# Kernel tuning notes

Measured on AMD Instinct MI355X. Metric: run time of the kernel, lower is better.

Reference implementation:

```python
import jax, jax.numpy as jnp
import numpy as np

V, D, NH, L, T, B = 32000, 1024, 16, 6, 1024, 2
HS = D // NH
EPS = 1e-5


def setup_inputs() -> dict:
    key = jax.random.key(0)
    ks = jax.random.split(key, 20)
    s = 0.02
    inp = {
        'tokens': jax.random.randint(ks[0], (B, T), 0, V),
        'tok_emb': jax.random.normal(ks[1], (V, D), jnp.float32) * s,
        'pos_emb': jax.random.normal(ks[2], (T, D), jnp.float32) * s,
        'Wq': jax.random.normal(ks[3], (L, D, NH, HS), jnp.float32) * s,
        'Wk': jax.random.normal(ks[4], (L, D, NH, HS), jnp.float32) * s,
        'Wv': jax.random.normal(ks[5], (L, D, NH, HS), jnp.float32) * s,
        'Wo': jax.random.normal(ks[6], (L, D, D), jnp.float32) * s,
        'bo': jnp.zeros((L, D), jnp.float32),
        'ln1_s': jnp.ones((L, D), jnp.float32),
        'ln1_b': jnp.zeros((L, D), jnp.float32),
        'ln2_s': jnp.ones((L, D), jnp.float32),
        'ln2_b': jnp.zeros((L, D), jnp.float32),
        'W1': jax.random.normal(ks[7], (L, D, 4 * D), jnp.float32) * s,
        'b1': jnp.zeros((L, 4 * D), jnp.float32),
        'W2': jax.random.normal(ks[8], (L, 4 * D, D), jnp.float32) * s,
        'b2': jnp.zeros((L, D), jnp.float32),
        'lnf_s': jnp.ones((D,), jnp.float32),
        'lnf_b': jnp.zeros((D,), jnp.float32),
        'Wlm': jax.random.normal(ks[9], (D, V), jnp.float32) * s,
        'blm': jnp.zeros((V,), jnp.float32),
    }
    return inp


def _layernorm(x, scale, bias):
    m = jnp.mean(x, axis=-1, keepdims=True)
    v = jnp.mean(jnp.square(x - m), axis=-1, keepdims=True)
    return (x - m) * jax.lax.rsqrt(v + EPS) * scale + bias


def reference(tokens, tok_emb, pos_emb, Wq, Wk, Wv, Wo, bo,
              ln1_s, ln1_b, ln2_s, ln2_b, W1, b1, W2, b2,
              lnf_s, lnf_b, Wlm, blm):
    x = tok_emb[tokens] + pos_emb[None, :, :]  # [B,T,D]
    causal = jnp.tril(jnp.ones((T, T), bool))
    scale = HS ** -0.5
    for l in range(L):
        h = _layernorm(x, ln1_s[l], ln1_b[l])
        q = jnp.einsum('btd,dhe->bhte', h, Wq[l])
        k = jnp.einsum('btd,dhe->bhte', h, Wk[l])
        v = jnp.einsum('btd,dhe->bhte', h, Wv[l])
        wei = jnp.einsum('bhqe,bhke->bhqk', q, k) * scale
        wei = jnp.where(causal, wei, -jnp.inf)
        wei = jax.nn.softmax(wei, axis=-1)
        attn = jnp.einsum('bhqk,bhke->bhqe', wei, v)  # [B,NH,T,HS]
        attn = attn.transpose(0, 2, 1, 3).reshape(B, T, D)
        x = x + attn @ Wo[l] + bo[l]
        h = _layernorm(x, ln2_s[l], ln2_b[l])
        x = x + jax.nn.relu(h @ W1[l] + b1[l]) @ W2[l] + b2[l]
    x = _layernorm(x, lnf_s, lnf_b)
    logits = x @ Wlm + blm  # [B,T,V]
    return logits
```

## Files before the change

### kernel.cpp

```cpp
#include <hip/hip_runtime.h>
#include <hip/hip_bf16.h>
#include <stdint.h>

#define L_LAYERS 6
#define D_MODEL  1024
#define N_HEAD   16
#define H_SZ     64
#define T_SEQ    1024
#define B_BATCH  2
#define M_ROWS   2048
#define V_VOCAB  32000

typedef __attribute__((ext_vector_type(8))) short bf16x8;
typedef __attribute__((ext_vector_type(4))) short bf16x4;
typedef __attribute__((ext_vector_type(4))) float floatx4;

static __device__ __forceinline__ short f2bf(float f) {
  __hip_bfloat16 h = __float2bfloat16(f);
  return *reinterpret_cast<short*>(&h);
}

static __device__ __forceinline__ void lds_cp16(const void* g, void* l) {
  __builtin_amdgcn_global_load_lds(
      (const __attribute__((address_space(1))) uint32_t*)g,
      (__attribute__((address_space(3))) uint32_t*)l, 16, 0, 0);
}

#define WVM(n) asm volatile("s_waitcnt vmcnt(" #n ")" ::: "memory")
#define BARR __builtin_amdgcn_s_barrier()

__global__ __launch_bounds__(256) void transpose_cvt(const float* __restrict__ in,
                                                     short* __restrict__ out,
                                                     int R, int C,
                                                     long in_stride, long out_stride) {
  in  += (size_t)blockIdx.z * in_stride;
  out += (size_t)blockIdx.z * out_stride;
  __shared__ float tile[64][65];
  int rt = blockIdx.x, ct = blockIdx.y;
  int tid = threadIdx.x;
  int r0 = tid >> 4;
  int c0 = (tid & 15) << 2;
  const float* ip = in + (size_t)(rt * 64) * C + ct * 64;
#pragma unroll
  for (int p = 0; p < 4; ++p) {
    int r = r0 + (p << 4);
    float4 v = *(const float4*)(ip + (size_t)r * C + c0);
    tile[r][c0] = v.x; tile[r][c0 + 1] = v.y; tile[r][c0 + 2] = v.z; tile[r][c0 + 3] = v.w;
  }
  __syncthreads();
  short* op = out + (size_t)(ct * 64) * R + rt * 64;
#pragma unroll
  for (int p = 0; p < 4; ++p) {
    int c = r0 + (p << 4);
    bf16x4 s;
    s.x = f2bf(tile[c0 + 0][c]);
    s.y = f2bf(tile[c0 + 1][c]);
    s.z = f2bf(tile[c0 + 2][c]);
    s.w = f2bf(tile[c0 + 3][c]);
    *(bf16x4*)(op + (size_t)c * R + c0) = s;
  }
}

__global__ __launch_bounds__(256) void embed_kernel(const int* __restrict__ tokens,
                                                    const float* __restrict__ tok_emb,
                                                    const float* __restrict__ pos_emb,
                                                    float* __restrict__ x) {
  int row = blockIdx.x;
  int t = row & 1023;
  int tok = tokens[row];
  int c = threadIdx.x << 2;
  float4 e = *(const float4*)(tok_emb + (size_t)tok * 1024 + c);
  float4 p = *(const float4*)(pos_emb + (size_t)t * 1024 + c);
  float4 rr; rr.x = e.x + p.x; rr.y = e.y + p.y; rr.z = e.z + p.z; rr.w = e.w + p.w;
  *(float4*)(x + (size_t)row * 1024 + c) = rr;
}

__global__ __launch_bounds__(256) void ln_kernel(const float* __restrict__ xin,
                                                 const float* __restrict__ sc,
                                                 const float* __restrict__ bi,
                                                 short* __restrict__ out) {
  int row = blockIdx.x, tid = threadIdx.x;
  int c = tid << 2;
  float4 v = *(const float4*)(xin + (size_t)row * 1024 + c);
  float s = v.x + v.y + v.z + v.w;
  float q = v.x * v.x + v.y * v.y + v.z * v.z + v.w * v.w;
#pragma unroll
  for (int off = 32; off > 0; off >>= 1) {
    s += __shfl_xor(s, off);
    q += __shfl_xor(q, off);
  }
  __shared__ float rs[4], rq[4];
  if ((tid & 63) == 0) { rs[tid >> 6] = s; rq[tid >> 6] = q; }
  __syncthreads();
  s = rs[0] + rs[1] + rs[2] + rs[3];
  q = rq[0] + rq[1] + rq[2] + rq[3];
  float mean = s * (1.f / 1024.f);
  float var = q * (1.f / 1024.f) - mean * mean;
  float rstd = rsqrtf(var + 1e-5f);
  float4 g = *(const float4*)(sc + c);
  float4 bb = *(const float4*)(bi + c);
  bf16x4 o4;
  o4.x = f2bf((v.x - mean) * rstd * g.x + bb.x);
  o4.y = f2bf((v.y - mean) * rstd * g.y + bb.y);
  o4.z = f2bf((v.z - mean) * rstd * g.z + bb.z);
  o4.w = f2bf((v.w - mean) * rstd * g.w + bb.w);
  *(bf16x4*)(out + (size_t)row * 1024 + c) = o4;
}

template <bool BIAS, bool RELU, bool RESID, bool OUTBF16>
__global__ __launch_bounds__(256) void gemm3_kernel(const short* __restrict__ A,
                                                    const short* __restrict__ Bt,
                                                    const float* __restrict__ bias,
                                                    const float* __restrict__ resid,
                                                    void* __restrict__ Cout,
                                                    int K, int N) {
  constexpr int ABY = 64 * 128;
  constexpr int BBY = 128 * 128;
  extern __shared__ char smem[];
  char* Asm = smem;
  char* Bsm = smem + 3 * ABY;
  const int NB = N >> 7;
  int nwg = 32 * NB;
  int bid = blockIdx.x;
  int wgid = (bid & 7) * (nwg >> 3) + (bid >> 3);
  int bn = wgid >> 5, bm = wgid & 31;
  int tid = threadIdx.x;
  int lane = tid & 63, w = tid >> 6;
  int lr = lane & 15, lg = lane >> 4;
  int wn = w & 1, wm = w >> 1;

  const floatx4 FZ = {0.f, 0.f, 0.f, 0.f};
  floatx4 acc[2][4];
#pragma unroll
  for (int m = 0; m < 2; ++m)
#pragma unroll
    for (int n = 0; n < 4; ++n) acc[m][n] = FZ;

  size_t aoff[2], boff[4];
  {
    int rr = tid >> 3;
    int g = (tid & 7) ^ (rr & 7);
#pragma unroll
    for (int i = 0; i < 2; ++i)
      aoff[i] = (size_t)(bm * 64 + i * 32 + rr) * K + g * 8;
#pragma unroll
    for (int i = 0; i < 4; ++i)
      boff[i] = (size_t)(bn * 128 + i * 32 + rr) * K + g * 8;
  }

#define STA3(b, k0)                                                        \
  _Pragma("unroll") for (int i = 0; i < 2; ++i)                            \
    lds_cp16(A + aoff[i] + (k0), Asm + (b) * ABY + i * 4096 + tid * 16);
#define STB3(b, k0)                                                        \
  _Pragma("unroll") for (int i = 0; i < 4; ++i)                            \
    lds_cp16(Bt + boff[i] + (k0), Bsm + (b) * BBY + i * 4096 + tid * 16);
#define LDA3(b, kh)                                                        \
  _Pragma("unroll") for (int f = 0; f < 2; ++f) {                          \
    int lrow = wm * 32 + f * 16 + lr;                                      \
    af[f] = *(const bf16x8*)(Asm + (b) * ABY + lrow * 128 +                \
                             (((((kh) << 2) + lg) ^ (lrow & 7)) << 4));    \
  }
#define LDB3(b, kh)                                                        \
  _Pragma("unroll") for (int n = 0; n < 4; ++n) {                          \
    int lcol = wn * 64 + n * 16 + lr;                                      \
    bfr[n] = *(const bf16x8*)(Bsm + (b) * BBY + lcol * 128 +               \
                              (((((kh) << 2) + lg) ^ (lcol & 7)) << 4));   \
  }
#define MFMA3                                                              \
  __builtin_amdgcn_s_setprio(1);                                           \
  _Pragma("unroll") for (int f = 0; f < 2; ++f)                            \
  _Pragma("unroll") for (int n = 0; n < 4; ++n)                            \
    acc[f][n] = __builtin_amdgcn_mfma_f32_16x16x32_bf16(af[f], bfr[n],     \
                                                        acc[f][n], 0, 0, 0);\
  __builtin_amdgcn_s_setprio(0);

  const int nt = K >> 6;
  STA3(0, 0); STB3(0, 0);
  STA3(1, 64); STB3(1, 64);
  WVM(6);
  BARR;

  int cbuf = 0, sbuf = 2;
  for (int t = 0; t < nt; ++t) {
    bf16x8 af[2], bfr[4];
    bool pre = (t + 2 < nt);
    int k2 = (t + 2) << 6;
    if (pre) { STA3(sbuf, k2); }
    LDA3(cbuf, 0); LDB3(cbuf, 0);
    MFMA3;
    if (pre) { STB3(sbuf, k2); }
    LDA3(cbuf, 1); LDB3(cbuf, 1);
    MFMA3;
    if (pre) { WVM(6); } else { WVM(0); }
    BARR;
    cbuf = (cbuf == 2) ? 0 : cbuf + 1;
    sbuf = (sbuf == 2) ? 0 : sbuf + 1;
  }

#pragma unroll
  for (int n = 0; n < 4; ++n) {
    int col = (bn << 7) + wn * 64 + (n << 4) + lr;
    float bv = 0.f;
    if (BIAS) bv = bias[col];
#pragma unroll
    for (int m = 0; m < 2; ++m) {
      int row0 = bm * 64 + wm * 32 + (m << 4) + (lg << 2);
#pragma unroll
      for (int r = 0; r < 4; ++r) {
        size_t idx = (size_t)(row0 + r) * N + col;
        float val = acc[m][n][r] + bv;
        if (RESID) val += resid[idx];
        if (RELU) val = fmaxf(val, 0.f);
        if (OUTBF16) ((short*)Cout)[idx] = f2bf(val);
        else ((float*)Cout)[idx] = val;
      }
    }
  }
#undef STA3
#undef STB3
#undef LDA3
#undef LDB3
#undef MFMA3
}

template <bool BIAS, bool OUTBF16>
__global__ __launch_bounds__(512) void gemm8_kernel(const short* __restrict__ A,
                                                    const short* __restrict__ Bt,
                                                    const float* __restrict__ bias,
                                                    void* __restrict__ Cout,
                                                    int K, int N) {
  extern __shared__ char smem[];
  char* Asm = smem;
  char* Bsm = smem + 65536;
  const int NB = N >> 8;
  int nwg = 8 * NB;
  int bid = blockIdx.x;
  int wgid = (bid & 7) * (nwg >> 3) + (bid >> 3);
  int bm = wgid & 7, bn = wgid >> 3;
  int tid = threadIdx.x;
  int lane = tid & 63, w = tid >> 6;
  int lr = lane & 15, lg = lane >> 4;
  int wm = w >> 2, wn = w & 3;

  const floatx4 FZ = {0.f, 0.f, 0.f, 0.f};
  floatx4 acc[8][4];
#pragma unroll
  for (int m = 0; m < 8; ++m)
#pragma unroll
    for (int n = 0; n < 4; ++n) acc[m][n] = FZ;

  size_t aoff[2][2], boff[4];
  {
    int rr = tid >> 3;
    int g = (tid & 7) ^ (rr & 7);
#pragma unroll
    for (int c = 0; c < 2; ++c)
#pragma unroll
      for (int i = 0; i < 2; ++i) {
        int lrow = i * 64 + rr;
        int grow = (lrow & 63) + ((lrow >> 6) << 7) + (c << 6);
        aoff[c][i] = (size_t)(bm * 256 + grow) * K + g * 8;
      }
#pragma unroll
    for (int i = 0; i < 4; ++i)
      boff[i] = (size_t)(bn * 256 + i * 64 + rr) * K + g * 8;
  }

  bf16x8 areg[4], breg[2][4];

#define LDA8(chunk, kh)                                                          \
  _Pragma("unroll") for (int f = 0; f < 4; ++f) {                                \
    int lrow = wm * 64 + f * 16 + lr;                                            \
    areg[f] = *(const bf16x8*)(Asm + buf * 32768 + (chunk) * 16384 + lrow * 128  \
                               + (((((kh) << 2) + lg) ^ (lrow & 7)) << 4));      \
  }
#define LDB8(kh)                                                                 \
  _Pragma("unroll") for (int n = 0; n < 4; ++n) {                                \
    int lcol = wn * 64 + n * 16 + lr;                                            \
    breg[kh][n] = *(const bf16x8*)(Bsm + buf * 32768 + lcol * 128                \
                                   + (((((kh) << 2) + lg) ^ (lcol & 7)) << 4));  \
  }
#define MFMA16(mh, kh)                                                           \
  __builtin_amdgcn_s_setprio(1);                                                 \
  _Pragma("unroll") for (int f = 0; f < 4; ++f)                                  \
  _Pragma("unroll") for (int n = 0; n < 4; ++n)                                  \
    acc[(mh) * 4 + f][n] = __builtin_amdgcn_mfma_f32_16x16x32_bf16(              \
        areg[f], breg[kh][n], acc[(mh) * 4 + f][n], 0, 0, 0);                    \
  __builtin_amdgcn_s_setprio(0);
#define STA8(chunk, dstbuf, k0)                                                  \
  _Pragma("unroll") for (int i = 0; i < 2; ++i)                                  \
    lds_cp16(A + aoff[chunk][i] + (k0),                                          \
             Asm + (dstbuf) * 32768 + (chunk) * 16384 + i * 8192 + tid * 16);
#define STB8(dstbuf, k0)                                                         \
  _Pragma("unroll") for (int i = 0; i < 4; ++i)                                  \
    lds_cp16(Bt + boff[i] + (k0),                                                \
             Bsm + (dstbuf) * 32768 + i * 8192 + tid * 16);

  const int nt = K >> 6;
  STA8(0, 0, 0); STB8(0, 0); STA8(1, 0, 0);
  WVM(2);
  BARR;

  int buf = 0;
  for (int t = 0; t < nt - 1; ++t) {
    int k1 = (t + 1) << 6;
    int ob = buf ^ 1;
    LDA8(0, 0); LDB8(0);
    STA8(0, ob, k1);
    BARR;
    MFMA16(0, 0);
    BARR;
    LDA8(0, 1); LDB8(1);
    STB8(ob, k1);
    WVM(6);
    BARR;
    MFMA16(0, 1);
    BARR;
    LDA8(1, 0);
    STA8(1, ob, k1);
    BARR;
    MFMA16(1, 0);
    BARR;
    LDA8(1, 1);
    WVM(2);
    BARR;
    MFMA16(1, 1);
    BARR;
    buf ^= 1;
  }
  LDA8(0, 0); LDB8(0);
  MFMA16(0, 0);
  LDA8(0, 1); LDB8(1);
  MFMA16(0, 1);
  WVM(0);
  BARR;
  LDA8(1, 0);
  MFMA16(1, 0);
  LDA8(1, 1);
  MFMA16(1, 1);

#pragma unroll
  for (int n = 0; n < 4; ++n) {
    int col = (bn << 8) + (wn << 6) + (n << 4) + lr;
    float bv = 0.f;
    if (BIAS) bv = bias[col];
#pragma unroll
    for (int m = 0; m < 8; ++m) {
      int row0 = (bm << 8) + (wm << 7) + (m << 4) + (lg << 2);
#pragma unroll
      for (int r = 0; r < 4; ++r) {
        size_t idx = (size_t)(row0 + r) * N + col;
        float val = acc[m][n][r] + bv;
        if (OUTBF16) ((short*)Cout)[idx] = f2bf(val);
        else ((float*)Cout)[idx] = val;
      }
    }
  }
#undef LDA8
#undef LDB8
#undef MFMA16
#undef STA8
#undef STB8
}

__global__ __launch_bounds__(256) void vt_kernel(const short* __restrict__ qkv,
                                                 short* __restrict__ vt) {
  int bh = blockIdx.x, tt = blockIdx.y;
  int b = bh >> 4, hh = bh & 15;
  __shared__ short tile[64][68];
  int tid = threadIdx.x;
  int r0 = tid >> 4;
  int c4 = (tid & 15) << 2;
  const short* ip = qkv + (size_t)((b << 10) + (tt << 6)) * 3072 + 2048 + (hh << 6);
#pragma unroll
  for (int p = 0; p < 4; ++p) {
    int t = r0 + (p << 4);
    bf16x4 v = *(const bf16x4*)(ip + (size_t)t * 3072 + c4);
    tile[t][c4] = v.x; tile[t][c4 + 1] = v.y; tile[t][c4 + 2] = v.z; tile[t][c4 + 3] = v.w;
  }
  __syncthreads();
  short* op = vt + (size_t)(bh << 6) * 1024 + (tt << 6);
#pragma unroll
  for (int p = 0; p < 4; ++p) {
    int e = r0 + (p << 4);
    bf16x4 sv;
    sv.x = tile[c4 + 0][e];
    sv.y = tile[c4 + 1][e];
    sv.z = tile[c4 + 2][e];
    sv.w = tile[c4 + 3][e];
    *(bf16x4*)(op + (size_t)e * 1024 + c4) = sv;
  }
}

__global__ __launch_bounds__(256) void attn_kernel(const short* __restrict__ qkv,
                                                   const short* __restrict__ vt,
                                                   short* __restrict__ out) {
  int bh = blockIdx.x;
  int qt = blockIdx.y;
  int b = bh >> 4, hh = bh & 15;
  int tid = threadIdx.x;
  int lane = tid & 63, w = tid >> 6;
  int lr = lane & 15, lg = lane >> 4;

  __shared__ short Ks[64 * 64];
  __shared__ short Vs[64 * 64];
  __shared__ short Ps[4][16 * 68];

  const floatx4 FZ = {0.f, 0.f, 0.f, 0.f};
  const short* qb = qkv + (size_t)((b << 10) + (qt << 6) + (w << 4) + lr) * 3072 + (hh << 6);
  bf16x8 qf0 = *(const bf16x8*)(qb + (lg << 3));
  bf16x8 qf1 = *(const bf16x8*)(qb + 32 + (lg << 3));

  floatx4 o[4];
  float mrun[4], lrun[4];
#pragma unroll
  for (int r = 0; r < 4; ++r) { o[r] = FZ; mrun[r] = -3e38f; lrun[r] = 0.f; }

  int sr = lane >> 3;
  int cb = (lane & 7) << 4;
  int csw = cb ^ (sr << 4);
  const short* kB = qkv + (size_t)(b << 10) * 3072 + 1024 + (hh << 6);
  const short* vB = vt + (size_t)(bh << 6) * 1024;

  for (int jt = 0; jt <= qt; ++jt) {
    __syncthreads();
#pragma unroll
    for (int j = 0; j < 2; ++j) {
      int ch = w * 2 + j;
      int row = (ch << 3) + sr;
      lds_cp16(kB + (size_t)((jt << 6) + row) * 3072 + (csw >> 1), (short*)Ks + (ch << 9));
      lds_cp16(vB + (size_t)row * 1024 + (jt << 6) + (csw >> 1), (short*)Vs + (ch << 9));
    }
    __syncthreads();

    const char* KsB = (const char*)Ks;
    const char* VsB = (const char*)Vs;
    floatx4 s[4];
#pragma unroll
    for (int f = 0; f < 4; ++f) {
      int rk = (f << 4) + lr;
      int sw = (rk & 7) << 4;
      bf16x8 kf0 = *(const bf16x8*)(KsB + rk * 128 + ((lg << 4) ^ sw));
      bf16x8 kf1 = *(const bf16x8*)(KsB + rk * 128 + ((64 + (lg << 4)) ^ sw));
      floatx4 t = __builtin_amdgcn_mfma_f32_16x16x32_bf16(qf0, kf0, FZ, 0, 0, 0);
      s[f] = __builtin_amdgcn_mfma_f32_16x16x32_bf16(qf1, kf1, t, 0, 0, 0);
    }

    float p[4][4], mt[4];
    bool diag = (jt == qt);
    int rowloc = (w << 4) + (lg << 2);
#pragma unroll
    for (int r = 0; r < 4; ++r) {
      float m = -3e38f;
#pragma unroll
      for (int f = 0; f < 4; ++f) {
        float sv = s[f][r] * 0.125f;
        if (diag && ((f << 4) + lr > rowloc + r)) sv = -3e38f;
        p[f][r] = sv;
        m = fmaxf(m, sv);
      }
      mt[r] = m;
    }
#pragma unroll
    for (int off = 1; off < 16; off <<= 1) {
#pragma unroll
      for (int r = 0; r < 4; ++r) mt[r] = fmaxf(mt[r], __shfl_xor(mt[r], off));
    }
    float corr[4], psum[4];
#pragma unroll
    for (int r = 0; r < 4; ++r) {
      float mnew = fmaxf(mrun[r], mt[r]);
      corr[r] = __expf(mrun[r] - mnew);
      mrun[r] = mnew;
      float ps = 0.f;
#pragma unroll
      for (int f = 0; f < 4; ++f) {
        float e = __expf(p[f][r] - mnew);
        p[f][r] = e;
        ps += e;
      }
      psum[r] = ps;
    }
#pragma unroll
    for (int off = 1; off < 16; off <<= 1) {
#pragma unroll
      for (int r = 0; r < 4; ++r) psum[r] += __shfl_xor(psum[r], off);
    }
    floatx4 cv;
#pragma unroll
    for (int r = 0; r < 4; ++r) { lrun[r] = lrun[r] * corr[r] + psum[r]; cv[r] = corr[r]; }
#pragma unroll
    for (int f = 0; f < 4; ++f) o[f] *= cv;

    char* PsB = (char*)&Ps[w][0];
#pragma unroll
    for (int f = 0; f < 4; ++f)
#pragma unroll
      for (int r = 0; r < 4; ++r)
        *(short*)(PsB + ((lg << 2) + r) * 136 + (((f << 4) + lr) << 1)) = f2bf(p[f][r]);

#pragma unroll
    for (int kk = 0; kk < 2; ++kk) {
      const char* pb = PsB + lr * 136 + (kk << 6) + (lg << 4);
      union { struct { bf16x4 lo, hi; } h2; bf16x8 v; } pu;
      pu.h2.lo = *(const bf16x4*)pb;
      pu.h2.hi = *(const bf16x4*)(pb + 8);
      bf16x8 pa = pu.v;
#pragma unroll
      for (int f = 0; f < 4; ++f) {
        int rv = (f << 4) + lr;
        int sw = (rv & 7) << 4;
        bf16x8 vf = *(const bf16x8*)(VsB + rv * 128 + ((((kk << 6)) + (lg << 4)) ^ sw));
        o[f] = __builtin_amdgcn_mfma_f32_16x16x32_bf16(pa, vf, o[f], 0, 0, 0);
      }
    }
  }

#pragma unroll
  for (int f = 0; f < 4; ++f) {
#pragma unroll
    for (int r = 0; r < 4; ++r) {
      int row = (qt << 6) + (w << 4) + (lg << 2) + r;
      int col = (hh << 6) + (f << 4) + lr;
      out[(size_t)((b << 10) + row) * 1024 + col] = f2bf(o[f][r] / lrun[r]);
    }
  }
}

extern "C" void kernel_launch(void* const* d_in, const int* in_sizes, int n_in,
                              void* d_out, int out_size, void* d_ws, size_t ws_size,
                              hipStream_t stream) {
  const int*   tokens  = (const int*)d_in[0];
  const float* tok_emb = (const float*)d_in[1];
  const float* pos_emb = (const float*)d_in[2];
  const float* Wq  = (const float*)d_in[3];
  const float* Wk  = (const float*)d_in[4];
  const float* Wv  = (const float*)d_in[5];
  const float* Wo  = (const float*)d_in[6];
  const float* bo  = (const float*)d_in[7];
  const float* ln1s = (const float*)d_in[8];
  const float* ln1b = (const float*)d_in[9];
  const float* ln2s = (const float*)d_in[10];
  const float* ln2b = (const float*)d_in[11];
  const float* W1  = (const float*)d_in[12];
  const float* b1  = (const float*)d_in[13];
  const float* W2  = (const float*)d_in[14];
  const float* b2  = (const float*)d_in[15];
  const float* lnfs = (const float*)d_in[16];
  const float* lnfb = (const float*)d_in[17];
  const float* Wlm = (const float*)d_in[18];
  const float* blm = (const float*)d_in[19];

  short* wqkvT = (short*)d_ws;
  short* woT   = wqkvT + (size_t)L_LAYERS * 3072 * 1024;
  short* w1T   = woT   + (size_t)L_LAYERS * 1024 * 1024;
  short* w2T   = w1T   + (size_t)L_LAYERS * 4096 * 1024;
  short* wlmT  = w2T   + (size_t)L_LAYERS * 1024 * 4096;
  float* x     = (float*)(wlmT + (size_t)V_VOCAB * 1024);
  short* h     = (short*)(x + (size_t)M_ROWS * 1024);
  short* qkv   = h + (size_t)M_ROWS * 1024;
  short* vtb   = qkv + (size_t)M_ROWS * 3072;
  short* attnb = vtb + (size_t)B_BATCH * N_HEAD * H_SZ * T_SEQ;
  short* mid   = attnb + (size_t)M_ROWS * 1024;

  dim3 blk(256, 1, 1);

  (void)hipFuncSetAttribute(reinterpret_cast<const void*>(&gemm8_kernel<true, false>),
                            hipFuncAttributeMaxDynamicSharedMemorySize, 131072);
  (void)hipFuncSetAttribute(reinterpret_cast<const void*>(&gemm3_kernel<false, false, false, true>),
                            hipFuncAttributeMaxDynamicSharedMemorySize, 73728);
  (void)hipFuncSetAttribute(reinterpret_cast<const void*>(&gemm3_kernel<true, false, true, false>),
                            hipFuncAttributeMaxDynamicSharedMemorySize, 73728);
  (void)hipFuncSetAttribute(reinterpret_cast<const void*>(&gemm3_kernel<true, true, false, true>),
                            hipFuncAttributeMaxDynamicSharedMemorySize, 73728);

  transpose_cvt<<<dim3(16, 16, 6), blk, 0, stream>>>(Wq, wqkvT,             1024, 1024, 1048576, 3072 * 1024);
  transpose_cvt<<<dim3(16, 16, 6), blk, 0, stream>>>(Wk, wqkvT + 1048576,   1024, 1024, 1048576, 3072 * 1024);
  transpose_cvt<<<dim3(16, 16, 6), blk, 0, stream>>>(Wv, wqkvT + 2097152,   1024, 1024, 1048576, 3072 * 1024);
  transpose_cvt<<<dim3(16, 16, 6), blk, 0, stream>>>(Wo, woT,               1024, 1024, 1048576, 1048576);
  transpose_cvt<<<dim3(16, 64, 6), blk, 0, stream>>>(W1, w1T,               1024, 4096, 4194304, 4194304);
  transpose_cvt<<<dim3(64, 16, 6), blk, 0, stream>>>(W2, w2T,               4096, 1024, 4194304, 4194304);
  transpose_cvt<<<dim3(16, 500, 1), blk, 0, stream>>>(Wlm, wlmT,            1024, V_VOCAB, 0, 0);

  embed_kernel<<<M_ROWS, blk, 0, stream>>>(tokens, tok_emb, pos_emb, x);

  for (int l = 0; l < L_LAYERS; ++l) {
    ln_kernel<<<M_ROWS, blk, 0, stream>>>(x, ln1s + l * 1024, ln1b + l * 1024, h);
    gemm3_kernel<false, false, false, true><<<32 * 24, blk, 73728, stream>>>(
        h, wqkvT + (size_t)l * 3072 * 1024, nullptr, nullptr, qkv, 1024, 3072);
    vt_kernel<<<dim3(32, 16), blk, 0, stream>>>(qkv, vtb);
    attn_kernel<<<dim3(32, 16), blk, 0, stream>>>(qkv, vtb, attnb);
    gemm3_kernel<true, false, true, false><<<32 * 8, blk, 73728, stream>>>(
        attnb, woT + (size_t)l * 1048576, bo + l * 1024, x, x, 1024, 1024);
    ln_kernel<<<M_ROWS, blk, 0, stream>>>(x, ln2s + l * 1024, ln2b + l * 1024, h);
    gemm3_kernel<true, true, false, true><<<32 * 32, blk, 73728, stream>>>(
        h, w1T + (size_t)l * 4194304, b1 + l * 4096, nullptr, mid, 1024, 4096);
    gemm3_kernel<true, false, true, false><<<32 * 8, blk, 73728, stream>>>(
        mid, w2T + (size_t)l * 4194304, b2 + l * 1024, x, x, 4096, 1024);
  }

  ln_kernel<<<M_ROWS, blk, 0, stream>>>(x, lnfs, lnfb, h);
  gemm8_kernel<true, false><<<dim3(8 * 125), dim3(512, 1, 1), 131072, stream>>>(
      h, wlmT, blm, (float*)d_out, 1024, V_VOCAB);
}
```

Before: 1.210 ms.

## Split-K narrow GEMMs, fuse residual reduce into layernorm, fold V transpose into QKV

The N=1024 GEMMs (Wo, W2), which previously launched only 256 workgroups, now use a two-way split-K kernel that writes fp32 partial sums. A new kernel adds both partials, the bias and the residual, then applies layernorm in one pass. Embedding is fused with the first layernorm, and the QKV GEMM epilogue writes V directly in transposed layout, which removes the separate transpose kernel. The GEMM K-tile is also halved to 32 to cut LDS use and raise occupancy. The cost is extra fp32 partial-buffer traffic and more barriers per unit of work.

```diff
diff --git a/kernel.cpp b/kernel.cpp
--- a/kernel.cpp
+++ b/kernel.cpp
@@ -61,27 +61,21 @@
   }
 }
 
-__global__ __launch_bounds__(256) void embed_kernel(const int* __restrict__ tokens,
-                                                    const float* __restrict__ tok_emb,
-                                                    const float* __restrict__ pos_emb,
-                                                    float* __restrict__ x) {
-  int row = blockIdx.x;
+__global__ __launch_bounds__(256) void embedln_kernel(const int* __restrict__ tokens,
+                                                      const float* __restrict__ tok_emb,
+                                                      const float* __restrict__ pos_emb,
+                                                      float* __restrict__ x,
+                                                      const float* __restrict__ sc,
+                                                      const float* __restrict__ bi,
+                                                      short* __restrict__ out) {
+  int row = blockIdx.x, tid = threadIdx.x;
   int t = row & 1023;
   int tok = tokens[row];
-  int c = threadIdx.x << 2;
+  int c = tid << 2;
   float4 e = *(const float4*)(tok_emb + (size_t)tok * 1024 + c);
   float4 p = *(const float4*)(pos_emb + (size_t)t * 1024 + c);
-  float4 rr; rr.x = e.x + p.x; rr.y = e.y + p.y; rr.z = e.z + p.z; rr.w = e.w + p.w;
-  *(float4*)(x + (size_t)row * 1024 + c) = rr;
-}
-
-__global__ __launch_bounds__(256) void ln_kernel(const float* __restrict__ xin,
-                                                 const float* __restrict__ sc,
-                                                 const float* __restrict__ bi,
-                                                 short* __restrict__ out) {
-  int row = blockIdx.x, tid = threadIdx.x;
-  int c = tid << 2;
-  float4 v = *(const float4*)(xin + (size_t)row * 1024 + c);
+  float4 v; v.x = e.x + p.x; v.y = e.y + p.y; v.z = e.z + p.z; v.w = e.w + p.w;
+  *(float4*)(x + (size_t)row * 1024 + c) = v;
   float s = v.x + v.y + v.z + v.w;
   float q = v.x * v.x + v.y * v.y + v.z * v.z + v.w * v.w;
 #pragma unroll
@@ -107,15 +101,59 @@
   *(bf16x4*)(out + (size_t)row * 1024 + c) = o4;
 }
 
-template <bool BIAS, bool RELU, bool RESID, bool OUTBF16>
-__global__ __launch_bounds__(256) void gemm3_kernel(const short* __restrict__ A,
-                                                    const short* __restrict__ Bt,
-                                                    const float* __restrict__ bias,
-                                                    const float* __restrict__ resid,
-                                                    void* __restrict__ Cout,
-                                                    int K, int N) {
-  constexpr int ABY = 64 * 128;
-  constexpr int BBY = 128 * 128;
+__global__ __launch_bounds__(256) void lnred_kernel(float* __restrict__ xio,
+                                                    const float* __restrict__ P0,
+                                                    const float* __restrict__ P1,
+                                                    const float* __restrict__ gb,
+                                                    const float* __restrict__ sc,
+                                                    const float* __restrict__ bi,
+                                                    short* __restrict__ out) {
+  int row = blockIdx.x, tid = threadIdx.x;
+  int c = tid << 2;
+  size_t base = (size_t)row * 1024 + c;
+  float4 v = *(const float4*)(xio + base);
+  float4 p0 = *(const float4*)(P0 + base);
+  float4 p1 = *(const float4*)(P1 + base);
+  float4 gv = *(const float4*)(gb + c);
+  v.x += p0.x + p1.x + gv.x;
+  v.y += p0.y + p1.y + gv.y;
+  v.z += p0.z + p1.z + gv.z;
+  v.w += p0.w + p1.w + gv.w;
+  *(float4*)(xio + base) = v;
+  float s = v.x + v.y + v.z + v.w;
+  float q = v.x * v.x + v.y * v.y + v.z * v.z + v.w * v.w;
+#pragma unroll
+  for (int off = 32; off > 0; off >>= 1) {
+    s += __shfl_xor(s, off);
+    q += __shfl_xor(q, off);
+  }
+  __shared__ float rs[4], rq[4];
+  if ((tid & 63) == 0) { rs[tid >> 6] = s; rq[tid >> 6] = q; }
+  __syncthreads();
+  s = rs[0] + rs[1] + rs[2] + rs[3];
+  q = rq[0] + rq[1] + rq[2] + rq[3];
+  float mean = s * (1.f / 1024.f);
+  float var = q * (1.f / 1024.f) - mean * mean;
+  float rstd = rsqrtf(var + 1e-5f);
+  float4 g = *(const float4*)(sc + c);
+  float4 bb = *(const float4*)(bi + c);
+  bf16x4 o4;
+  o4.x = f2bf((v.x - mean) * rstd * g.x + bb.x);
+  o4.y = f2bf((v.y - mean) * rstd * g.y + bb.y);
+  o4.z = f2bf((v.z - mean) * rstd * g.z + bb.z);
+  o4.w = f2bf((v.w - mean) * rstd * g.w + bb.w);
+  *(bf16x4*)(out + (size_t)row * 1024 + c) = o4;
+}
+
+template <bool BIAS, bool RELU, bool OUTBF16, bool VSPLIT>
+__global__ __launch_bounds__(256, 4) void gemm3_kernel(const short* __restrict__ A,
+                                                       const short* __restrict__ Bt,
+                                                       const float* __restrict__ bias,
+                                                       void* __restrict__ Cout,
+                                                       short* __restrict__ vtb,
+                                                       int K, int N) {
+  constexpr int ABY = 64 * 64;
+  constexpr int BBY = 128 * 64;
   extern __shared__ char smem[];
   char* Asm = smem;
   char* Bsm = smem + 3 * ABY;
@@ -136,35 +174,31 @@
 #pragma unroll
     for (int n = 0; n < 4; ++n) acc[m][n] = FZ;
 
-  size_t aoff[2], boff[4];
+  size_t aoff, boff[2];
   {
-    int rr = tid >> 3;
-    int g = (tid & 7) ^ (rr & 7);
+    int rr = tid >> 2;
+    int g = (tid & 3) ^ (rr & 3);
+    aoff = (size_t)(bm * 64 + rr) * K + g * 8;
 #pragma unroll
     for (int i = 0; i < 2; ++i)
-      aoff[i] = (size_t)(bm * 64 + i * 32 + rr) * K + g * 8;
-#pragma unroll
-    for (int i = 0; i < 4; ++i)
-      boff[i] = (size_t)(bn * 128 + i * 32 + rr) * K + g * 8;
-  }
-
-#define STA3(b, k0)                                                        \
+      boff[i] = (size_t)(bn * 128 + i * 64 + rr) * K + g * 8;
+  }
+
+#define STA3(b, k0) lds_cp16(A + aoff + (k0), Asm + (b) * ABY + tid * 16);
+#define STB3(b, k0)                                                        \
   _Pragma("unroll") for (int i = 0; i < 2; ++i)                            \
-    lds_cp16(A + aoff[i] + (k0), Asm + (b) * ABY + i * 4096 + tid * 16);
-#define STB3(b, k0)                                                        \
-  _Pragma("unroll") for (int i = 0; i < 4; ++i)                            \
     lds_cp16(Bt + boff[i] + (k0), Bsm + (b) * BBY + i * 4096 + tid * 16);
-#define LDA3(b, kh)                                                        \
+#define LDA3(b)                                                            \
   _Pragma("unroll") for (int f = 0; f < 2; ++f) {                          \
     int lrow = wm * 32 + f * 16 + lr;                                      \
-    af[f] = *(const bf16x8*)(Asm + (b) * ABY + lrow * 128 +                \
-                             (((((kh) << 2) + lg) ^ (lrow & 7)) << 4));    \
-  }
-#define LDB3(b, kh)                                                        \
+    af[f] = *(const bf16x8*)(Asm + (b) * ABY + lrow * 64 +                 \
+                             ((lg ^ (lrow & 3)) << 4));                    \
+  }
+#define LDB3(b)                                                            \
   _Pragma("unroll") for (int n = 0; n < 4; ++n) {                          \
     int lcol = wn * 64 + n * 16 + lr;                                      \
-    bfr[n] = *(const bf16x8*)(Bsm + (b) * BBY + lcol * 128 +               \
-                              (((((kh) << 2) + lg) ^ (lcol & 7)) << 4));   \
+    bfr[n] = *(const bf16x8*)(Bsm + (b) * BBY + lcol * 64 +                \
+                              ((lg ^ (lcol & 3)) << 4));                   \
   }
 #define MFMA3                                                              \
   __builtin_amdgcn_s_setprio(1);                                           \
@@ -174,24 +208,21 @@
                                                         acc[f][n], 0, 0, 0);\
   __builtin_amdgcn_s_setprio(0);
 
-  const int nt = K >> 6;
+  const int nt = K >> 5;
   STA3(0, 0); STB3(0, 0);
-  STA3(1, 64); STB3(1, 64);
-  WVM(6);
+  STA3(1, 32); STB3(1, 32);
+  WVM(3);
   BARR;
 
   int cbuf = 0, sbuf = 2;
   for (int t = 0; t < nt; ++t) {
     bf16x8 af[2], bfr[4];
     bool pre = (t + 2 < nt);
-    int k2 = (t + 2) << 6;
-    if (pre) { STA3(sbuf, k2); }
-    LDA3(cbuf, 0); LDB3(cbuf, 0);
+    int k2 = (t + 2) << 5;
+    if (pre) { STA3(sbuf, k2); STB3(sbuf, k2); }
+    LDA3(cbuf); LDB3(cbuf);
     MFMA3;
-    if (pre) { STB3(sbuf, k2); }
-    LDA3(cbuf, 1); LDB3(cbuf, 1);
-    MFMA3;
-    if (pre) { WVM(6); } else { WVM(0); }
+    if (pre) { WVM(3); } else { WVM(0); }
     BARR;
     cbuf = (cbuf == 2) ? 0 : cbuf + 1;
     sbuf = (sbuf == 2) ? 0 : sbuf + 1;
@@ -205,15 +236,127 @@
 #pragma unroll
     for (int m = 0; m < 2; ++m) {
       int row0 = bm * 64 + wm * 32 + (m << 4) + (lg << 2);
-#pragma unroll
-      for (int r = 0; r < 4; ++r) {
-        size_t idx = (size_t)(row0 + r) * N + col;
-        float val = acc[m][n][r] + bv;
-        if (RESID) val += resid[idx];
-        if (RELU) val = fmaxf(val, 0.f);
-        if (OUTBF16) ((short*)Cout)[idx] = f2bf(val);
-        else ((float*)Cout)[idx] = val;
+      if (VSPLIT && col >= 2048) {
+        int hc = col - 2048;
+        int b = row0 >> 10, t4 = row0 & 1023;
+        ushort4 pk;
+        pk.x = (unsigned short)f2bf(acc[m][n][0]);
+        pk.y = (unsigned short)f2bf(acc[m][n][1]);
+        pk.z = (unsigned short)f2bf(acc[m][n][2]);
+        pk.w = (unsigned short)f2bf(acc[m][n][3]);
+        *(ushort4*)(vtb + ((size_t)(((b << 4) + (hc >> 6)) << 6) + (hc & 63)) * 1024 + t4) = pk;
+      } else {
+#pragma unroll
+        for (int r = 0; r < 4; ++r) {
+          size_t idx = (size_t)(row0 + r) * N + col;
+          float val = acc[m][n][r] + bv;
+          if (RELU) val = fmaxf(val, 0.f);
+          if (OUTBF16) ((short*)Cout)[idx] = f2bf(val);
+          else ((float*)Cout)[idx] = val;
+        }
       }
+    }
+  }
+#undef STA3
+#undef STB3
+#undef LDA3
+#undef LDB3
+#undef MFMA3
+}
+
+__global__ __launch_bounds__(256, 4) void gemm3sk_kernel(const short* __restrict__ A,
+                                                         const short* __restrict__ Bt,
+                                                         float* __restrict__ Pout,
+                                                         int K, int N) {
+  constexpr int ABY = 64 * 64;
+  constexpr int BBY = 128 * 64;
+  extern __shared__ char smem[];
+  char* Asm = smem;
+  char* Bsm = smem + 3 * ABY;
+  const int NB = N >> 7;
+  int nwg = 64 * NB;
+  int bid = blockIdx.x;
+  int wgid = (bid & 7) * (nwg >> 3) + (bid >> 3);
+  int half = wgid >= (nwg >> 1);
+  int w2 = wgid - half * (nwg >> 1);
+  int bn = w2 >> 5, bm = w2 & 31;
+  int kbase = half * (K >> 1);
+  Pout += (size_t)half * M_ROWS * N;
+  int tid = threadIdx.x;
+  int lane = tid & 63, w = tid >> 6;
+  int lr = lane & 15, lg = lane >> 4;
+  int wn = w & 1, wm = w >> 1;
+
+  const floatx4 FZ = {0.f, 0.f, 0.f, 0.f};
+  floatx4 acc[2][4];
+#pragma unroll
+  for (int m = 0; m < 2; ++m)
+#pragma unroll
+    for (int n = 0; n < 4; ++n) acc[m][n] = FZ;
+
+  size_t aoff, boff[2];
+  {
+    int rr = tid >> 2;
+    int g = (tid & 3) ^ (rr & 3);
+    aoff = (size_t)(bm * 64 + rr) * K + kbase + g * 8;
+#pragma unroll
+    for (int i = 0; i < 2; ++i)
+      boff[i] = (size_t)(bn * 128 + i * 64 + rr) * K + kbase + g * 8;
+  }
+
+#define STA3(b, k0) lds_cp16(A + aoff + (k0), Asm + (b) * ABY + tid * 16);
+#define STB3(b, k0)                                                        \
+  _Pragma("unroll") for (int i = 0; i < 2; ++i)                            \
+    lds_cp16(Bt + boff[i] + (k0), Bsm + (b) * BBY + i * 4096 + tid * 16);
+#define LDA3(b)                                                            \
+  _Pragma("unroll") for (int f = 0; f < 2; ++f) {                          \
+    int lrow = wm * 32 + f * 16 + lr;                                      \
+    af[f] = *(const bf16x8*)(Asm + (b) * ABY + lrow * 64 +                 \
+                             ((lg ^ (lrow & 3)) << 4));                    \
+  }
+#define LDB3(b)                                                            \
+  _Pragma("unroll") for (int n = 0; n < 4; ++n) {                          \
+    int lcol = wn * 64 + n * 16 + lr;                                      \
+    bfr[n] = *(const bf16x8*)(Bsm + (b) * BBY + lcol * 64 +                \
+                              ((lg ^ (lcol & 3)) << 4));                   \
+  }
+#define MFMA3                                                              \
+  __builtin_amdgcn_s_setprio(1);                                           \
+  _Pragma("unroll") for (int f = 0; f < 2; ++f)                            \
+  _Pragma("unroll") for (int n = 0; n < 4; ++n)                            \
+    acc[f][n] = __builtin_amdgcn_mfma_f32_16x16x32_bf16(af[f], bfr[n],     \
+                                                        acc[f][n], 0, 0, 0);\
+  __builtin_amdgcn_s_setprio(0);
+
+  const int nt = (K >> 1) >> 5;
+  STA3(0, 0); STB3(0, 0);
+  STA3(1, 32); STB3(1, 32);
+  WVM(3);
+  BARR;
+
+  int cbuf = 0, sbuf = 2;
+  for (int t = 0; t < nt; ++t) {
+    bf16x8 af[2], bfr[4];
+    bool pre = (t + 2 < nt);
+    int k2 = (t + 2) << 5;
+    if (pre) { STA3(sbuf, k2); STB3(sbuf, k2); }
+    LDA3(cbuf); LDB3(cbuf);
+    MFMA3;
+    if (pre) { WVM(3); } else { WVM(0); }
+    BARR;
+    cbuf = (cbuf == 2) ? 0 : cbuf + 1;
+    sbuf = (sbuf == 2) ? 0 : sbuf + 1;
+  }
+
+#pragma unroll
+  for (int n = 0; n < 4; ++n) {
+    int col = (bn << 7) + wn * 64 + (n << 4) + lr;
+#pragma unroll
+    for (int m = 0; m < 2; ++m) {
+      int row0 = bm * 64 + wm * 32 + (m << 4) + (lg << 2);
+#pragma unroll
+      for (int r = 0; r < 4; ++r)
+        Pout[(size_t)(row0 + r) * N + col] = acc[m][n][r];
     }
   }
 #undef STA3
@@ -361,35 +504,6 @@
 #undef MFMA16
 #undef STA8
 #undef STB8
-}
-
-__global__ __launch_bounds__(256) void vt_kernel(const short* __restrict__ qkv,
-                                                 short* __restrict__ vt) {
-  int bh = blockIdx.x, tt = blockIdx.y;
-  int b = bh >> 4, hh = bh & 15;
-  __shared__ short tile[64][68];
-  int tid = threadIdx.x;
-  int r0 = tid >> 4;
-  int c4 = (tid & 15) << 2;
-  const short* ip = qkv + (size_t)((b << 10) + (tt << 6)) * 3072 + 2048 + (hh << 6);
-#pragma unroll
-  for (int p = 0; p < 4; ++p) {
-    int t = r0 + (p << 4);
-    bf16x4 v = *(const bf16x4*)(ip + (size_t)t * 3072 + c4);
-    tile[t][c4] = v.x; tile[t][c4 + 1] = v.y; tile[t][c4 + 2] = v.z; tile[t][c4 + 3] = v.w;
-  }
-  __syncthreads();
-  short* op = vt + (size_t)(bh << 6) * 1024 + (tt << 6);
-#pragma unroll
-  for (int p = 0; p < 4; ++p) {
-    int e = r0 + (p << 4);
-    bf16x4 sv;
-    sv.x = tile[c4 + 0][e];
-    sv.y = tile[c4 + 1][e];
-    sv.z = tile[c4 + 2][e];
-    sv.w = tile[c4 + 3][e];
-    *(bf16x4*)(op + (size_t)e * 1024 + c4) = sv;
-  }
 }
 
 __global__ __launch_bounds__(256) void attn_kernel(const short* __restrict__ qkv,
@@ -562,17 +676,19 @@
   short* vtb   = qkv + (size_t)M_ROWS * 3072;
   short* attnb = vtb + (size_t)B_BATCH * N_HEAD * H_SZ * T_SEQ;
   short* mid   = attnb + (size_t)M_ROWS * 1024;
+  float* psum  = (float*)(mid + (size_t)M_ROWS * 4096);
+  float* psum1 = psum + (size_t)M_ROWS * 1024;
 
   dim3 blk(256, 1, 1);
 
   (void)hipFuncSetAttribute(reinterpret_cast<const void*>(&gemm8_kernel<true, false>),
                             hipFuncAttributeMaxDynamicSharedMemorySize, 131072);
-  (void)hipFuncSetAttribute(reinterpret_cast<const void*>(&gemm3_kernel<false, false, false, true>),
-                            hipFuncAttributeMaxDynamicSharedMemorySize, 73728);
-  (void)hipFuncSetAttribute(reinterpret_cast<const void*>(&gemm3_kernel<true, false, true, false>),
-                            hipFuncAttributeMaxDynamicSharedMemorySize, 73728);
-  (void)hipFuncSetAttribute(reinterpret_cast<const void*>(&gemm3_kernel<true, true, false, true>),
-                            hipFuncAttributeMaxDynamicSharedMemorySize, 73728);
+  (void)hipFuncSetAttribute(reinterpret_cast<const void*>(&gemm3_kernel<false, false, true, true>),
+                            hipFuncAttributeMaxDynamicSharedMemorySize, 36864);
+  (void)hipFuncSetAttribute(reinterpret_cast<const void*>(&gemm3_kernel<true, true, true, false>),
+                            hipFuncAttributeMaxDynamicSharedMemorySize, 36864);
+  (void)hipFuncSetAttribute(reinterpret_cast<const void*>(&gemm3sk_kernel),
+                            hipFuncAttributeMaxDynamicSharedMemorySize, 36864);
 
   transpose_cvt<<<dim3(16, 16, 6), blk, 0, stream>>>(Wq, wqkvT,             1024, 1024, 1048576, 3072 * 1024);
   transpose_cvt<<<dim3(16, 16, 6), blk, 0, stream>>>(Wk, wqkvT + 1048576,   1024, 1024, 1048576, 3072 * 1024);
@@ -582,24 +698,28 @@
   transpose_cvt<<<dim3(64, 16, 6), blk, 0, stream>>>(W2, w2T,               4096, 1024, 4194304, 4194304);
   transpose_cvt<<<dim3(16, 500, 1), blk, 0, stream>>>(Wlm, wlmT,            1024, V_VOCAB, 0, 0);
 
-  embed_kernel<<<M_ROWS, blk, 0, stream>>>(tokens, tok_emb, pos_emb, x);
+  embedln_kernel<<<M_ROWS, blk, 0, stream>>>(tokens, tok_emb, pos_emb, x, ln1s, ln1b, h);
 
   for (int l = 0; l < L_LAYERS; ++l) {
-    ln_kernel<<<M_ROWS, blk, 0, stream>>>(x, ln1s + l * 1024, ln1b + l * 1024, h);
-    gemm3_kernel<false, false, false, true><<<32 * 24, blk, 73728, stream>>>(
-        h, wqkvT + (size_t)l * 3072 * 1024, nullptr, nullptr, qkv, 1024, 3072);
-    vt_kernel<<<dim3(32, 16), blk, 0, stream>>>(qkv, vtb);
+    if (l > 0) {
+      lnred_kernel<<<M_ROWS, blk, 0, stream>>>(x, psum, psum1, b2 + (l - 1) * 1024,
+                                               ln1s + l * 1024, ln1b + l * 1024, h);
+    }
+    gemm3_kernel<false, false, true, true><<<32 * 24, blk, 36864, stream>>>(
+        h, wqkvT + (size_t)l * 3072 * 1024, nullptr, qkv, vtb, 1024, 3072);
     attn_kernel<<<dim3(32, 16), blk, 0, stream>>>(qkv, vtb, attnb);
-    gemm3_kernel<true, false, true, false><<<32 * 8, blk, 73728, stream>>>(
-        attnb, woT + (size_t)l * 1048576, bo + l * 1024, x, x, 1024, 1024);
-    ln_kernel<<<M_ROWS, blk, 0, stream>>>(x, ln2s + l * 1024, ln2b + l * 1024, h);
-    gemm3_kernel<true, true, false, true><<<32 * 32, blk, 73728, stream>>>(
-        h, w1T + (size_t)l * 4194304, b1 + l * 4096, nullptr, mid, 1024, 4096);
-    gemm3_kernel<true, false, true, false><<<32 * 8, blk, 73728, stream>>>(
-        mid, w2T + (size_t)l * 4194304, b2 + l * 1024, x, x, 4096, 1024);
-  }
-
-  ln_kernel<<<M_ROWS, blk, 0, stream>>>(x, lnfs, lnfb, h);
+    gemm3sk_kernel<<<64 * 8, blk, 36864, stream>>>(
+        attnb, woT + (size_t)l * 1048576, psum, 1024, 1024);
+    lnred_kernel<<<M_ROWS, blk, 0, stream>>>(x, psum, psum1, bo + l * 1024,
+                                             ln2s + l * 1024, ln2b + l * 1024, h);
+    gemm3_kernel<true, true, true, false><<<32 * 32, blk, 36864, stream>>>(
+        h, w1T + (size_t)l * 4194304, b1 + l * 4096, mid, nullptr, 1024, 4096);
+    gemm3sk_kernel<<<64 * 8, blk, 36864, stream>>>(
+        mid, w2T + (size_t)l * 4194304, psum, 4096, 1024);
+  }
+
+  lnred_kernel<<<M_ROWS, blk, 0, stream>>>(x, psum, psum1, b2 + 5 * 1024,
+                                           lnfs, lnfb, h);
   gemm8_kernel<true, false><<<dim3(8 * 125), dim3(512, 1, 1), 131072, stream>>>(
       h, wlmT, blm, (float*)d_out, 1024, V_VOCAB);
 }
```

Measured after the change: 1.278 ms. 5.6% more time.
